# Kernel optimization log

Hardware: AMD Instinct MI355X
Metric: run time of the kernel (lower is better)

Reference implementation:

```python
import jax, jax.numpy as jnp
import numpy as np

B, C, H, W = 32, 384, 64, 64
M, R = 64, 16  # token_count, factor_r


def setup_inputs() -> dict:
    key = jax.random.key(0)
    k1, k2, k3, k4 = jax.random.split(key, 4)
    x = jax.random.normal(k1, (B, C, H, W), dtype=jnp.float32)
    # 1x1 conv == per-pixel linear map C -> R
    Vw = jax.random.normal(k2, (R, C), dtype=jnp.float32) * (1.0 / np.sqrt(C))
    Vb = jax.random.normal(k3, (R,), dtype=jnp.float32) * 0.01
    U = jax.random.normal(k4, (M, R), dtype=jnp.float32) * 0.02
    return {"x": x, "Vw": Vw, "Vb": Vb, "U": U}


def reference(x, Vw, Vb, U):
    b, c, h, w = x.shape
    n = h * w
    x_flat = x.reshape(b, c, n)                       # [B,C,N]
    # 1x1 conv projection: [B,R,N]
    V = jnp.einsum('rc,bcn->brn', Vw, x_flat) + Vb[None, :, None]
    # low-rank bilinear logits: [B,M,N]
    L = jnp.einsum('mr,brn->bmn', U, V)
    # softmax over token dim (axis=1), matching F.softmax(L, dim=1)
    S = jax.nn.softmax(L, axis=1)
    # pooled tokens: [B,C,M]
    T = jnp.einsum('bcn,bmn->bcm', x_flat, S)
    return (T, S)
```

## Files before the change

kernel.cpp:

```cpp
#include <hip/hip_runtime.h>
#include <hip/hip_bf16.h>

#define B_ 32
#define C_ 384
#define N_ 4096
#define M_ 64
#define R_ 16

typedef __attribute__((ext_vector_type(8))) short short8;
typedef __attribute__((ext_vector_type(4))) float f32x4;
typedef __attribute__((ext_vector_type(4))) int i32x4;

static __device__ __forceinline__ unsigned short f2bf(float f) {
    union { float f; unsigned u; } v; v.f = f;
    unsigned r = v.u + 0x7fffu + ((v.u >> 16) & 1u);
    return (unsigned short)(r >> 16);
}

__global__ __launch_bounds__(256) void k_w2(
    const float* __restrict__ Vw, const float* __restrict__ Vb,
    const float* __restrict__ U, unsigned short* __restrict__ W2,
    float* __restrict__ b2)
{
    __shared__ float vws[16 * 384];
    __shared__ float vbs[16];
    const int t = threadIdx.x;

    #pragma unroll
    for (int j = 0; j < 6; ++j)
        ((float4*)vws)[t + j * 256] = ((const float4*)Vw)[t + j * 256];
    if (t < 16) vbs[t] = Vb[t];
    __syncthreads();

    const int m  = blockIdx.x * 8 + (t >> 5);
    const int cg = t & 31;
    float u[R_];
    #pragma unroll
    for (int r = 0; r < R_; ++r) u[r] = U[m * R_ + r];
    if (cg == 0) {
        float a = 0.f;
        #pragma unroll
        for (int r = 0; r < R_; ++r) a = fmaf(u[r], vbs[r], a);
        b2[m] = a;
    }
    #pragma unroll
    for (int j = 0; j < 6; ++j) {
        const int c = cg * 2 + j * 64;
        float a0 = 0.f, a1 = 0.f;
        #pragma unroll
        for (int r = 0; r < R_; ++r) {
            float2 vv = *(const float2*)(vws + r * C_ + c);
            a0 = fmaf(u[r], vv.x, a0);
            a1 = fmaf(u[r], vv.y, a1);
        }
        unsigned pk = (unsigned)f2bf(a0) | ((unsigned)f2bf(a1) << 16);
        *(unsigned*)&W2[m * C_ + c] = pk;
    }
}

__global__ __launch_bounds__(256, 2) void k_logits_softmax(
    const float* __restrict__ x, const unsigned short* __restrict__ W2,
    const float* __restrict__ b2, float* __restrict__ S)
{
    __shared__ unsigned short w2s[64][392];
    __shared__ unsigned short xts[128][72];
    __shared__ float b2s[64];

    const int t = threadIdx.x;

    #pragma unroll
    for (int j = 0; j < 12; ++j) {
        int idx = t + j * 256;
        int m = idx / 48, c8 = idx % 48;
        *(i32x4*)&w2s[m][c8 * 8] = ((const i32x4*)W2)[idx];
    }
    if (t < 64) b2s[t] = b2[t];

    const int b    = blockIdx.x >> 5;
    const int n0   = (blockIdx.x & 31) * 128;
    const int lane = t & 63, q = lane >> 4, col = lane & 15;
    const int w    = t >> 6;

    f32x4 acc[4][2];
    #pragma unroll
    for (int mt = 0; mt < 4; ++mt)
        #pragma unroll
        for (int nt = 0; nt < 2; ++nt)
            acc[mt][nt] = (f32x4){0.f, 0.f, 0.f, 0.f};

    const float* xbase = x + (size_t)(b * C_) * N_ + n0 + 2 * lane;

    for (int kc = 0; kc < 12; ++kc) {
        unsigned wA[4], wB[4];
        const float* xp = xbase + (size_t)(kc * 32 + w * 8) * N_;
        #pragma unroll
        for (int i = 0; i < 8; ++i) {
            float2 v = *(const float2*)(xp + (size_t)i * N_);
            unsigned ba = f2bf(v.x), bb = f2bf(v.y);
            if ((i & 1) == 0) { wA[i >> 1] = ba;        wB[i >> 1] = bb; }
            else              { wA[i >> 1] |= ba << 16; wB[i >> 1] |= bb << 16; }
        }
        __syncthreads();
        {
            const int nl = 2 * lane;
            i32x4 pa = {(int)wA[0], (int)wA[1], (int)wA[2], (int)wA[3]};
            i32x4 pb = {(int)wB[0], (int)wB[1], (int)wB[2], (int)wB[3]};
            *(i32x4*)&xts[nl][w * 8]     = pa;
            *(i32x4*)&xts[nl + 1][w * 8] = pb;
        }
        __syncthreads();

        short8 af[4], bfr[2];
        #pragma unroll
        for (int mt = 0; mt < 4; ++mt)
            af[mt] = *(const short8*)&w2s[mt * 16 + col][kc * 32 + q * 8];
        #pragma unroll
        for (int nt = 0; nt < 2; ++nt)
            bfr[nt] = *(const short8*)&xts[w * 32 + nt * 16 + col][q * 8];
        #pragma unroll
        for (int mt = 0; mt < 4; ++mt)
            #pragma unroll
            for (int nt = 0; nt < 2; ++nt)
                acc[mt][nt] = __builtin_amdgcn_mfma_f32_16x16x32_bf16(
                    af[mt], bfr[nt], acc[mt][nt], 0, 0, 0);
    }

    float bias[4][4];
    #pragma unroll
    for (int mt = 0; mt < 4; ++mt)
        #pragma unroll
        for (int r = 0; r < 4; ++r)
            bias[mt][r] = b2s[mt * 16 + q * 4 + r];

    float* Sb = S + (size_t)(b * M_) * N_ + n0 + w * 32 + col;
    #pragma unroll
    for (int nt = 0; nt < 2; ++nt) {
        float mx = -3.4e38f;
        #pragma unroll
        for (int mt = 0; mt < 4; ++mt)
            #pragma unroll
            for (int r = 0; r < 4; ++r) {
                float v = acc[mt][nt][r] + bias[mt][r];
                acc[mt][nt][r] = v;
                mx = fmaxf(mx, v);
            }
        mx = fmaxf(mx, __shfl_xor(mx, 16, 64));
        mx = fmaxf(mx, __shfl_xor(mx, 32, 64));
        float sm = 0.f;
        #pragma unroll
        for (int mt = 0; mt < 4; ++mt)
            #pragma unroll
            for (int r = 0; r < 4; ++r) {
                float e = __expf(acc[mt][nt][r] - mx);
                acc[mt][nt][r] = e;
                sm += e;
            }
        sm += __shfl_xor(sm, 16, 64);
        sm += __shfl_xor(sm, 32, 64);
        const float inv = 1.0f / sm;
        #pragma unroll
        for (int mt = 0; mt < 4; ++mt)
            #pragma unroll
            for (int r = 0; r < 4; ++r)
                Sb[(size_t)(mt * 16 + q * 4 + r) * N_ + nt * 16] = acc[mt][nt][r] * inv;
    }
}

__global__ __launch_bounds__(256, 4) void k_pool2(
    const float* __restrict__ x, const float* __restrict__ S,
    float* __restrict__ T)
{
    __shared__ unsigned short xls[128][72];
    __shared__ unsigned short sls[64][72];

    const int t  = threadIdx.x;
    const int ct = blockIdx.x;
    const int b  = blockIdx.y;
    const int nq = blockIdx.z;
    const int c0 = ct * 128;

    const float* xb = x + (size_t)(b * C_ + c0) * N_ + nq * 512;
    const float* sb = S + (size_t)(b * M_) * N_ + nq * 512;

    const int lane = t & 63, q = lane >> 4, col = lane & 15;
    const int w    = t >> 6;

    f32x4 acc[2][4];
    #pragma unroll
    for (int i = 0; i < 2; ++i)
        #pragma unroll
        for (int mt = 0; mt < 4; ++mt) acc[i][mt] = (f32x4){0.f, 0.f, 0.f, 0.f};

    for (int kc = 0; kc < 8; ++kc) {
        float4 xv[8], sv[4];
        #pragma unroll
        for (int j = 0; j < 8; ++j) {
            int idx = t + j * 256;
            int row = idx >> 4, cc = idx & 15;
            xv[j] = *(const float4*)(xb + (size_t)row * N_ + kc * 64 + cc * 4);
        }
        #pragma unroll
        for (int j = 0; j < 4; ++j) {
            int idx = t + j * 256;
            int row = idx >> 4, cc = idx & 15;
            sv[j] = *(const float4*)(sb + (size_t)row * N_ + kc * 64 + cc * 4);
        }
        __syncthreads();
        #pragma unroll
        for (int j = 0; j < 8; ++j) {
            int idx = t + j * 256;
            int row = idx >> 4, cc = idx & 15;
            int2 p;
            p.x = (int)((unsigned)f2bf(xv[j].x) | ((unsigned)f2bf(xv[j].y) << 16));
            p.y = (int)((unsigned)f2bf(xv[j].z) | ((unsigned)f2bf(xv[j].w) << 16));
            *(int2*)&xls[row][cc * 4] = p;
        }
        #pragma unroll
        for (int j = 0; j < 4; ++j) {
            int idx = t + j * 256;
            int row = idx >> 4, cc = idx & 15;
            int2 p;
            p.x = (int)((unsigned)f2bf(sv[j].x) | ((unsigned)f2bf(sv[j].y) << 16));
            p.y = (int)((unsigned)f2bf(sv[j].z) | ((unsigned)f2bf(sv[j].w) << 16));
            *(int2*)&sls[row][cc * 4] = p;
        }
        __syncthreads();

        #pragma unroll
        for (int ks = 0; ks < 2; ++ks) {
            short8 af[2];
            #pragma unroll
            for (int i = 0; i < 2; ++i)
                af[i] = *(const short8*)&xls[w * 32 + i * 16 + col][ks * 32 + q * 8];
            #pragma unroll
            for (int mt = 0; mt < 4; ++mt) {
                short8 bfr = *(const short8*)&sls[mt * 16 + col][ks * 32 + q * 8];
                #pragma unroll
                for (int i = 0; i < 2; ++i)
                    acc[i][mt] = __builtin_amdgcn_mfma_f32_16x16x32_bf16(
                        af[i], bfr, acc[i][mt], 0, 0, 0);
            }
        }
        __syncthreads();
    }

    float* Tb = T + (size_t)b * C_ * M_ + (size_t)c0 * M_;
    #pragma unroll
    for (int i = 0; i < 2; ++i)
        #pragma unroll
        for (int mt = 0; mt < 4; ++mt)
            #pragma unroll
            for (int r = 0; r < 4; ++r)
                atomicAdd(&Tb[(size_t)(w * 32 + i * 16 + q * 4 + r) * M_ + mt * 16 + col],
                          acc[i][mt][r]);
}

extern "C" void kernel_launch(void* const* d_in, const int* in_sizes, int n_in,
                              void* d_out, int out_size, void* d_ws, size_t ws_size,
                              hipStream_t stream) {
    const float* x  = (const float*)d_in[0];
    const float* Vw = (const float*)d_in[1];
    const float* Vb = (const float*)d_in[2];
    const float* U  = (const float*)d_in[3];
    float* T = (float*)d_out;
    float* S = (float*)d_out + (size_t)B_ * C_ * M_;

    unsigned short* W2 = (unsigned short*)d_ws;
    float* b2 = (float*)((char*)d_ws + 64 * 384 * 2);

    hipMemsetAsync(T, 0, (size_t)B_ * C_ * M_ * sizeof(float), stream);
    k_w2<<<dim3(8), dim3(256), 0, stream>>>(Vw, Vb, U, W2, b2);
    k_logits_softmax<<<dim3(32 * 32), dim3(256), 0, stream>>>(x, W2, b2, S);
    k_pool2<<<dim3(3, 32, 8), dim3(256), 0, stream>>>(x, S, T);
}
```

Before: 337.4 us.

## Fuse logits-softmax and pooling into one kernel keeping x tile in LDS

Merges the logits+softmax kernel and the pooling kernel into a single 512-thread kernel. Each block handles one batch and a 512-column slice of N in 128-column chunks, with the bf16 x tile kept in swizzled LDS and reused for the pooling MFMA, so x is read from HBM once instead of twice and S is not re-read. It adds register double-buffered prefetch of x, a cross-wave softmax reduction through shared memory, and keeps W2 fragments in registers. The risks are a large LDS footprint (about 100KB of x tile) that limits occupancy, and a grid of only 256 blocks with many barriers per block.

After: 318.5 us. 1.06x faster.

```diff
diff --git a/kernel.cpp b/kernel.cpp
--- a/kernel.cpp
+++ b/kernel.cpp
@@ -58,201 +58,188 @@
     }
 }
 
-__global__ __launch_bounds__(256, 2) void k_logits_softmax(
+__global__ __launch_bounds__(512, 2) void k_fused(
     const float* __restrict__ x, const unsigned short* __restrict__ W2,
-    const float* __restrict__ b2, float* __restrict__ S)
+    const float* __restrict__ b2g, float* __restrict__ S, float* __restrict__ T)
 {
-    __shared__ unsigned short w2s[64][392];
-    __shared__ unsigned short xts[128][72];
-    __shared__ float b2s[64];
-
-    const int t = threadIdx.x;
-
-    #pragma unroll
-    for (int j = 0; j < 12; ++j) {
-        int idx = t + j * 256;
-        int m = idx / 48, c8 = idx % 48;
-        *(i32x4*)&w2s[m][c8 * 8] = ((const i32x4*)W2)[idx];
-    }
-    if (t < 64) b2s[t] = b2[t];
-
-    const int b    = blockIdx.x >> 5;
-    const int n0   = (blockIdx.x & 31) * 128;
-    const int lane = t & 63, q = lane >> 4, col = lane & 15;
+    __shared__ unsigned short xcn[C_ * 128];
+    __shared__ union {
+        unsigned short xts[128][68];
+        unsigned short slds[M_ * 128];
+    } uu;
+    __shared__ float wred[2][4][128];
+
+    const int t    = threadIdx.x;
+    const int lane = t & 63;
+    const int col  = lane & 15;
+    const int q    = lane >> 4;
     const int w    = t >> 6;
-
-    f32x4 acc[4][2];
-    #pragma unroll
-    for (int mt = 0; mt < 4; ++mt)
-        #pragma unroll
-        for (int nt = 0; nt < 2; ++nt)
-            acc[mt][nt] = (f32x4){0.f, 0.f, 0.f, 0.f};
-
-    const float* xbase = x + (size_t)(b * C_) * N_ + n0 + 2 * lane;
-
-    for (int kc = 0; kc < 12; ++kc) {
-        unsigned wA[4], wB[4];
-        const float* xp = xbase + (size_t)(kc * 32 + w * 8) * N_;
-        #pragma unroll
-        for (int i = 0; i < 8; ++i) {
-            float2 v = *(const float2*)(xp + (size_t)i * N_);
-            unsigned ba = f2bf(v.x), bb = f2bf(v.y);
-            if ((i & 1) == 0) { wA[i >> 1] = ba;        wB[i >> 1] = bb; }
-            else              { wA[i >> 1] |= ba << 16; wB[i >> 1] |= bb << 16; }
-        }
-        __syncthreads();
-        {
-            const int nl = 2 * lane;
-            i32x4 pa = {(int)wA[0], (int)wA[1], (int)wA[2], (int)wA[3]};
-            i32x4 pb = {(int)wB[0], (int)wB[1], (int)wB[2], (int)wB[3]};
-            *(i32x4*)&xts[nl][w * 8]     = pa;
-            *(i32x4*)&xts[nl + 1][w * 8] = pb;
-        }
-        __syncthreads();
-
-        short8 af[4], bfr[2];
+    const int g    = w >> 1;
+    const int h    = w & 1;
+
+    const int b  = blockIdx.x >> 3;
+    const int nq = blockIdx.x & 7;
+
+    short8 af1[12];
+    #pragma unroll
+    for (int kk = 0; kk < 12; ++kk)
+        af1[kk] = *(const short8*)(W2 + (g * 16 + col) * C_ + kk * 32 + q * 8);
+
+    float bias[4];
+    #pragma unroll
+    for (int r = 0; r < 4; ++r) bias[r] = b2g[g * 16 + q * 4 + r];
+
+    f32x4 acc2[3][4];
+    #pragma unroll
+    for (int ci = 0; ci < 3; ++ci)
+        #pragma unroll
+        for (int mt = 0; mt < 4; ++mt) acc2[ci][mt] = (f32x4){0.f, 0.f, 0.f, 0.f};
+
+    const float* xb = x + (size_t)b * C_ * N_ + nq * 512 + 2 * lane;
+
+    float2 xv[2][8];
+    auto issue = [&](float2 (&dst)[8], int sub_, int kc_) {
+        const float* xp = xb + (size_t)(kc_ * 64 + w * 8) * N_ + sub_ * 128;
+        #pragma unroll
+        for (int i = 0; i < 8; ++i)
+            dst[i] = *(const float2*)(xp + (size_t)i * N_);
+    };
+
+    issue(xv[0], 0, 0);
+
+    for (int sub = 0; sub < 4; ++sub) {
+        f32x4 acc1[4];
+        #pragma unroll
+        for (int nt = 0; nt < 4; ++nt) acc1[nt] = (f32x4){0.f, 0.f, 0.f, 0.f};
+
+        #pragma unroll
+        for (int kc = 0; kc < 6; ++kc) {
+            if (kc < 5) issue(xv[(kc + 1) & 1], sub, kc + 1);
+            {
+                float2 (&v)[8] = xv[kc & 1];
+                unsigned short bx[8], by[8];
+                #pragma unroll
+                for (int i = 0; i < 8; ++i) { bx[i] = f2bf(v[i].x); by[i] = f2bf(v[i].y); }
+                #pragma unroll
+                for (int i = 0; i < 8; ++i) {
+                    int c = kc * 64 + w * 8 + i;
+                    unsigned pk = (unsigned)bx[i] | ((unsigned)by[i] << 16);
+                    *(unsigned*)((char*)xcn + c * 256 + ((lane * 4) ^ ((c & 7) << 4))) = pk;
+                }
+                i32x4 pa, pb;
+                #pragma unroll
+                for (int j = 0; j < 4; ++j) {
+                    pa[j] = (int)((unsigned)bx[2 * j] | ((unsigned)bx[2 * j + 1] << 16));
+                    pb[j] = (int)((unsigned)by[2 * j] | ((unsigned)by[2 * j + 1] << 16));
+                }
+                *(i32x4*)&uu.xts[2 * lane][w * 8]     = pa;
+                *(i32x4*)&uu.xts[2 * lane + 1][w * 8] = pb;
+            }
+            __syncthreads();
+            #pragma unroll
+            for (int ks = 0; ks < 2; ++ks) {
+                short8 bfr[4];
+                #pragma unroll
+                for (int nt = 0; nt < 4; ++nt)
+                    bfr[nt] = *(const short8*)&uu.xts[h * 64 + nt * 16 + col][ks * 32 + q * 8];
+                #pragma unroll
+                for (int nt = 0; nt < 4; ++nt)
+                    acc1[nt] = __builtin_amdgcn_mfma_f32_16x16x32_bf16(
+                        af1[kc * 2 + ks], bfr[nt], acc1[nt], 0, 0, 0);
+            }
+            __syncthreads();
+        }
+
+        #pragma unroll
+        for (int nt = 0; nt < 4; ++nt) {
+            float mx = -3.4e38f;
+            #pragma unroll
+            for (int r = 0; r < 4; ++r) {
+                float vv = acc1[nt][r] + bias[r];
+                acc1[nt][r] = vv;
+                mx = fmaxf(mx, vv);
+            }
+            mx = fmaxf(mx, __shfl_xor(mx, 16, 64));
+            mx = fmaxf(mx, __shfl_xor(mx, 32, 64));
+            if (q == 0) wred[0][g][h * 64 + nt * 16 + col] = mx;
+        }
+        __syncthreads();
+        #pragma unroll
+        for (int nt = 0; nt < 4; ++nt) {
+            int n = h * 64 + nt * 16 + col;
+            float gm = fmaxf(fmaxf(wred[0][0][n], wred[0][1][n]),
+                             fmaxf(wred[0][2][n], wred[0][3][n]));
+            float s = 0.f;
+            #pragma unroll
+            for (int r = 0; r < 4; ++r) {
+                float e = __expf(acc1[nt][r] - gm);
+                acc1[nt][r] = e;
+                s += e;
+            }
+            s += __shfl_xor(s, 16, 64);
+            s += __shfl_xor(s, 32, 64);
+            if (q == 0) wred[1][g][n] = s;
+        }
+        __syncthreads();
+        float inv_[4];
+        #pragma unroll
+        for (int nt = 0; nt < 4; ++nt) {
+            int n = h * 64 + nt * 16 + col;
+            float ts = (wred[1][0][n] + wred[1][1][n]) + (wred[1][2][n] + wred[1][3][n]);
+            inv_[nt] = 1.0f / ts;
+        }
+
+        if (sub < 3) issue(xv[0], sub + 1, 0);
+
+        float* Sp = S + (size_t)(b * M_ + g * 16 + q * 4) * N_ + nq * 512 + sub * 128;
+        #pragma unroll
+        for (int nt = 0; nt < 4; ++nt) {
+            int n = h * 64 + nt * 16 + col;
+            #pragma unroll
+            for (int r = 0; r < 4; ++r) {
+                float p = acc1[nt][r] * inv_[nt];
+                Sp[(size_t)r * N_ + n] = p;
+                int m = g * 16 + q * 4 + r;
+                *(unsigned short*)((char*)uu.slds + m * 256 + ((2 * n) ^ ((m & 7) << 4))) = f2bf(p);
+            }
+        }
+        __syncthreads();
+
+        #pragma unroll
+        for (int ks = 0; ks < 4; ++ks) {
+            short8 a2[3], bsf[4];
+            #pragma unroll
+            for (int ci = 0; ci < 3; ++ci) {
+                int c = w * 48 + ci * 16 + col;
+                a2[ci] = *(const short8*)((char*)xcn + c * 256 +
+                                          ((ks * 64 + q * 16) ^ ((c & 7) << 4)));
+            }
+            #pragma unroll
+            for (int mt = 0; mt < 4; ++mt) {
+                int m = mt * 16 + col;
+                bsf[mt] = *(const short8*)((char*)uu.slds + m * 256 +
+                                           ((ks * 64 + q * 16) ^ ((m & 7) << 4)));
+            }
+            #pragma unroll
+            for (int ci = 0; ci < 3; ++ci)
+                #pragma unroll
+                for (int mt = 0; mt < 4; ++mt)
+                    acc2[ci][mt] = __builtin_amdgcn_mfma_f32_16x16x32_bf16(
+                        a2[ci], bsf[mt], acc2[ci][mt], 0, 0, 0);
+        }
+        __syncthreads();
+    }
+
+    float* Tb = T + (size_t)b * C_ * M_;
+    #pragma unroll
+    for (int ci = 0; ci < 3; ++ci) {
+        int c = w * 48 + ci * 16 + q * 4;
         #pragma unroll
         for (int mt = 0; mt < 4; ++mt)
-            af[mt] = *(const short8*)&w2s[mt * 16 + col][kc * 32 + q * 8];
-        #pragma unroll
-        for (int nt = 0; nt < 2; ++nt)
-            bfr[nt] = *(const short8*)&xts[w * 32 + nt * 16 + col][q * 8];
-        #pragma unroll
-        for (int mt = 0; mt < 4; ++mt)
-            #pragma unroll
-            for (int nt = 0; nt < 2; ++nt)
-                acc[mt][nt] = __builtin_amdgcn_mfma_f32_16x16x32_bf16(
-                    af[mt], bfr[nt], acc[mt][nt], 0, 0, 0);
-    }
-
-    float bias[4][4];
-    #pragma unroll
-    for (int mt = 0; mt < 4; ++mt)
-        #pragma unroll
-        for (int r = 0; r < 4; ++r)
-            bias[mt][r] = b2s[mt * 16 + q * 4 + r];
-
-    float* Sb = S + (size_t)(b * M_) * N_ + n0 + w * 32 + col;
-    #pragma unroll
-    for (int nt = 0; nt < 2; ++nt) {
-        float mx = -3.4e38f;
-        #pragma unroll
-        for (int mt = 0; mt < 4; ++mt)
-            #pragma unroll
-            for (int r = 0; r < 4; ++r) {
-                float v = acc[mt][nt][r] + bias[mt][r];
-                acc[mt][nt][r] = v;
-                mx = fmaxf(mx, v);
-            }
-        mx = fmaxf(mx, __shfl_xor(mx, 16, 64));
-        mx = fmaxf(mx, __shfl_xor(mx, 32, 64));
-        float sm = 0.f;
-        #pragma unroll
-        for (int mt = 0; mt < 4; ++mt)
-            #pragma unroll
-            for (int r = 0; r < 4; ++r) {
-                float e = __expf(acc[mt][nt][r] - mx);
-                acc[mt][nt][r] = e;
-                sm += e;
-            }
-        sm += __shfl_xor(sm, 16, 64);
-        sm += __shfl_xor(sm, 32, 64);
-        const float inv = 1.0f / sm;
-        #pragma unroll
-        for (int mt = 0; mt < 4; ++mt)
             #pragma unroll
             for (int r = 0; r < 4; ++r)
-                Sb[(size_t)(mt * 16 + q * 4 + r) * N_ + nt * 16] = acc[mt][nt][r] * inv;
-    }
-}
-
-__global__ __launch_bounds__(256, 4) void k_pool2(
-    const float* __restrict__ x, const float* __restrict__ S,
-    float* __restrict__ T)
-{
-    __shared__ unsigned short xls[128][72];
-    __shared__ unsigned short sls[64][72];
-
-    const int t  = threadIdx.x;
-    const int ct = blockIdx.x;
-    const int b  = blockIdx.y;
-    const int nq = blockIdx.z;
-    const int c0 = ct * 128;
-
-    const float* xb = x + (size_t)(b * C_ + c0) * N_ + nq * 512;
-    const float* sb = S + (size_t)(b * M_) * N_ + nq * 512;
-
-    const int lane = t & 63, q = lane >> 4, col = lane & 15;
-    const int w    = t >> 6;
-
-    f32x4 acc[2][4];
-    #pragma unroll
-    for (int i = 0; i < 2; ++i)
-        #pragma unroll
-        for (int mt = 0; mt < 4; ++mt) acc[i][mt] = (f32x4){0.f, 0.f, 0.f, 0.f};
-
-    for (int kc = 0; kc < 8; ++kc) {
-        float4 xv[8], sv[4];
-        #pragma unroll
-        for (int j = 0; j < 8; ++j) {
-            int idx = t + j * 256;
-            int row = idx >> 4, cc = idx & 15;
-            xv[j] = *(const float4*)(xb + (size_t)row * N_ + kc * 64 + cc * 4);
-        }
-        #pragma unroll
-        for (int j = 0; j < 4; ++j) {
-            int idx = t + j * 256;
-            int row = idx >> 4, cc = idx & 15;
-            sv[j] = *(const float4*)(sb + (size_t)row * N_ + kc * 64 + cc * 4);
-        }
-        __syncthreads();
-        #pragma unroll
-        for (int j = 0; j < 8; ++j) {
-            int idx = t + j * 256;
-            int row = idx >> 4, cc = idx & 15;
-            int2 p;
-            p.x = (int)((unsigned)f2bf(xv[j].x) | ((unsigned)f2bf(xv[j].y) << 16));
-            p.y = (int)((unsigned)f2bf(xv[j].z) | ((unsigned)f2bf(xv[j].w) << 16));
-            *(int2*)&xls[row][cc * 4] = p;
-        }
-        #pragma unroll
-        for (int j = 0; j < 4; ++j) {
-            int idx = t + j * 256;
-            int row = idx >> 4, cc = idx & 15;
-            int2 p;
-            p.x = (int)((unsigned)f2bf(sv[j].x) | ((unsigned)f2bf(sv[j].y) << 16));
-            p.y = (int)((unsigned)f2bf(sv[j].z) | ((unsigned)f2bf(sv[j].w) << 16));
-            *(int2*)&sls[row][cc * 4] = p;
-        }
-        __syncthreads();
-
-        #pragma unroll
-        for (int ks = 0; ks < 2; ++ks) {
-            short8 af[2];
-            #pragma unroll
-            for (int i = 0; i < 2; ++i)
-                af[i] = *(const short8*)&xls[w * 32 + i * 16 + col][ks * 32 + q * 8];
-            #pragma unroll
-            for (int mt = 0; mt < 4; ++mt) {
-                short8 bfr = *(const short8*)&sls[mt * 16 + col][ks * 32 + q * 8];
-                #pragma unroll
-                for (int i = 0; i < 2; ++i)
-                    acc[i][mt] = __builtin_amdgcn_mfma_f32_16x16x32_bf16(
-                        af[i], bfr, acc[i][mt], 0, 0, 0);
-            }
-        }
-        __syncthreads();
-    }
-
-    float* Tb = T + (size_t)b * C_ * M_ + (size_t)c0 * M_;
-    #pragma unroll
-    for (int i = 0; i < 2; ++i)
-        #pragma unroll
-        for (int mt = 0; mt < 4; ++mt)
-            #pragma unroll
-            for (int r = 0; r < 4; ++r)
-                atomicAdd(&Tb[(size_t)(w * 32 + i * 16 + q * 4 + r) * M_ + mt * 16 + col],
-                          acc[i][mt][r]);
+                atomicAdd(&Tb[(size_t)(c + r) * M_ + mt * 16 + col], acc2[ci][mt][r]);
+    }
 }
 
 extern "C" void kernel_launch(void* const* d_in, const int* in_sizes, int n_in,
@@ -270,6 +257,5 @@
 
     hipMemsetAsync(T, 0, (size_t)B_ * C_ * M_ * sizeof(float), stream);
     k_w2<<<dim3(8), dim3(256), 0, stream>>>(Vw, Vb, U, W2, b2);
-    k_logits_softmax<<<dim3(32 * 32), dim3(256), 0, stream>>>(x, W2, b2, S);
-    k_pool2<<<dim3(3, 32, 8), dim3(256), 0, stream>>>(x, S, T);
-}
+    k_fused<<<dim3(256), dim3(512), 0, stream>>>(x, W2, b2, S, T);
+}
```
